# Kernel optimization log

Measured on AMD Instinct MI355X. Metric: run time of the kernel, lower is better.

The kernel has to match this reference:

```python
import jax, jax.numpy as jnp
import numpy as np
from jax import lax

N_QUBITS = 8
N_BLOCKS = 5

_H = jnp.array([[1.0, 1.0], [1.0, -1.0]], dtype=jnp.complex64) / np.sqrt(2.0).astype(np.float32)
# torchquantum PauliY.diagonalizing_gates = [Z, S, H] applied in order -> matrix H @ S @ Z = H @ diag(1, -1j)
_YROT = _H @ jnp.diag(jnp.array([1.0, -1j], dtype=jnp.complex64))


def apply_gate(st, U, wires):
    # st: [N, 2, 2, ..., 2] (n_qubits trailing axes); U: [2^k, 2^k]
    k = len(wires)
    axes = [w + 1 for w in wires]
    s = jnp.moveaxis(st, axes, list(range(1, k + 1)))
    shp = s.shape
    s = s.reshape(shp[0], 2 ** k, -1)
    s = jnp.einsum('ij,bjr->bir', U, s)
    return jnp.moveaxis(s.reshape(shp), list(range(1, k + 1)), axes)


def u3_mat(th, ph, lam):
    c = jnp.cos(0.5 * th).astype(jnp.complex64)
    s = jnp.sin(0.5 * th).astype(jnp.complex64)
    el = jnp.exp(1j * lam)
    ep = jnp.exp(1j * ph)
    return jnp.stack([jnp.stack([c, -el * s]), jnp.stack([ep * s, ep * el * c])])


def cu3_mat(th, ph, lam):
    M = jnp.eye(4, dtype=jnp.complex64)
    return M.at[2:, 2:].set(u3_mat(th, ph, lam))


def z_expvals(st):
    # <Z_w> for every wire from marginal probabilities
    n = st.ndim - 1
    mag = st.real ** 2 + st.imag ** 2
    outs = []
    for w in range(n):
        axes = tuple(a for a in range(1, n + 1) if a != w + 1)
        p = mag.sum(axes)  # [N, 2]
        outs.append(p[:, 0] - p[:, 1])
    return jnp.stack(outs, axis=1)


def quantum_conv(x, conv_w, conv_b, u3_params, cu3_params, fc_w, fc_b):
    n = N_QUBITS
    B, C, H, W = x.shape
    y = lax.conv_general_dilated(x, conv_w, (1, 1), 'SAME',
                                 dimension_numbers=('NCHW', 'OIHW', 'NCHW'))
    y = y + conv_b[None, :, None, None]
    ang = y.transpose(0, 2, 3, 1).reshape(-1, n)  # [B*H*W, n_qubits]
    Npx = ang.shape[0]
    # RY(theta)|0> encoding: product state of [cos(t/2), sin(t/2)] per wire
    c = jnp.cos(0.5 * ang)
    s = jnp.sin(0.5 * ang)
    st = jnp.stack([c[:, 0], s[:, 0]], axis=1).astype(jnp.complex64)
    for w in range(1, n):
        q = jnp.stack([c[:, w], s[:, w]], axis=1).astype(jnp.complex64)
        st = (st[:, :, None] * q[:, None, :]).reshape(Npx, -1)
    st = st.reshape((Npx,) + (2,) * n)
    # U3CU3Layer0: per block, U3 on each wire then circular CU3 ring
    for b in range(N_BLOCKS):
        for w in range(n):
            st = apply_gate(st, u3_mat(u3_params[b, w, 0], u3_params[b, w, 1], u3_params[b, w, 2]), [w])
        for w in range(n):
            st = apply_gate(st, cu3_mat(cu3_params[b, w, 0], cu3_params[b, w, 1], cu3_params[b, w, 2]), [w, (w + 1) % n])
    # MeasureAll(Z), then MeasureAll(X) and MeasureAll(Y) which MUTATE the device
    # state with their diagonalizing gates (torchquantum semantics)
    mz = z_expvals(st)
    for w in range(n):
        st = apply_gate(st, _H, [w])
    mx = z_expvals(st)
    for w in range(n):
        st = apply_gate(st, _YROT, [w])
    my = z_expvals(st)
    meas = jnp.concatenate([mz, mx, my], axis=1)  # [B*H*W, 3*n]
    out = meas @ fc_w.T + fc_b
    return out.reshape(B, H, W, -1).transpose(0, 3, 1, 2)


def setup_inputs() -> dict:
    key = jax.random.key(0)
    ks = jax.random.split(key, 7)
    n, cin, cout = N_QUBITS, 16, 32
    x = jax.random.normal(ks[0], (4, cin, 64, 64), dtype=jnp.float32)
    conv_w = jax.random.normal(ks[1], (n, cin, 3, 3), dtype=jnp.float32) / np.sqrt(cin * 9)
    conv_b = jax.random.normal(ks[2], (n,), dtype=jnp.float32) * 0.01
    u3_params = jax.random.uniform(ks[3], (N_BLOCKS, n, 3), dtype=jnp.float32, minval=-np.pi, maxval=np.pi)
    cu3_params = jax.random.uniform(ks[4], (N_BLOCKS, n, 3), dtype=jnp.float32, minval=-np.pi, maxval=np.pi)
    fc_w = jax.random.normal(ks[5], (cout, 3 * n), dtype=jnp.float32) / np.sqrt(3 * n)
    fc_b = jax.random.normal(ks[6], (cout,), dtype=jnp.float32) * 0.01
    return {'x': x, 'conv_w': conv_w, 'conv_b': conv_b, 'u3_params': u3_params,
            'cu3_params': cu3_params, 'fc_w': fc_w, 'fc_b': fc_b}


def reference(x, conv_w, conv_b, u3_params, cu3_params, fc_w, fc_b):
    return quantum_conv(x, conv_w, conv_b, u3_params, cu3_params, fc_w, fc_b)
```

## Files before the change

### kernel.cpp

```cpp
#include <hip/hip_runtime.h>

typedef float v2f __attribute__((ext_vector_type(2)));

template<int C>
__device__ __forceinline__ float dppmov(float x) {
  return __int_as_float(__builtin_amdgcn_update_dpp(0, __float_as_int(x), C, 0xF, 0xF, true));
}
template<int IMM>
__device__ __forceinline__ float dswz(float x) {
  return __int_as_float(__builtin_amdgcn_ds_swizzle(__float_as_int(x), IMM));
}
__device__ __forceinline__ float bperm(float x, int a) {
  return __int_as_float(__builtin_amdgcn_ds_bpermute(a, __float_as_int(x)));
}
template<int M>
__device__ __forceinline__ float bfly(float x) {
  if constexpr (M == 1)      return dppmov<0xB1>(x);
  else if constexpr (M == 2) return dppmov<0x4E>(x);
  else if constexpr (M == 3) return dppmov<0x1B>(x);
  else if constexpr (M == 8) return dppmov<0x128>(x);
  else                       return dswz<0x101F>(x);
}
template<int M>
__device__ __forceinline__ v2f bfly2(v2f v) {
  v2f o; o.x = bfly<M>(v.x); o.y = bfly<M>(v.y); return o;
}
__device__ __forceinline__ v2f sp(float s) { v2f v; v.x = s; v.y = s; return v; }
__device__ __forceinline__ v2f vfma(v2f a, v2f b, v2f c) {
  return __builtin_elementwise_fma(a, b, c);
}

template<int M, int CM>
__device__ __forceinline__ void crossG(v2f Sr[16], v2f Si[16],
    const float* g, int lane) {
  const bool hi = (lane & M) != 0;
  float fr, fi, gr, gi;
  if constexpr (CM == 0) {
    fr = hi ? g[6] : g[0]; fi = hi ? g[7] : g[1];
    gr = hi ? g[4] : g[2]; gi = hi ? g[5] : g[3];
  } else {
    const bool ct = (lane & CM) != 0;
    float f0r = hi ? g[6]  : g[0],  f0i = hi ? g[7]  : g[1];
    float g0r = hi ? g[4]  : g[2],  g0i = hi ? g[5]  : g[3];
    float f1r = hi ? g[14] : g[8],  f1i = hi ? g[15] : g[9];
    float g1r = hi ? g[12] : g[10], g1i = hi ? g[13] : g[11];
    fr = ct ? f1r : f0r; fi = ct ? f1i : f0i;
    gr = ct ? g1r : g0r; gi = ct ? g1i : g0i;
  }
  v2f vfr = sp(fr), vfi = sp(fi), vgr = sp(gr), vgi = sp(gi);
  v2f vfiN = sp(-fi), vgiN = sp(-gi);
#pragma unroll
  for (int r = 0; r < 16; ++r) {
    v2f pR = bfly2<M>(Sr[r]);
    v2f pI = bfly2<M>(Si[r]);
    v2f nR = vfma(vgiN, pI, vfma(vgr, pR, vfma(vfiN, Si[r], vfr * Sr[r])));
    v2f nI = vfma(vgi,  pR, vfma(vgr, pI, vfma(vfi,  Sr[r], vfr * Si[r])));
    Sr[r] = nR; Si[r] = nI;
  }
}

__device__ __forceinline__ void mixP(v2f& x0r, v2f& x0i, v2f& x1r, v2f& x1i,
    float m0r, float m0i, float m1r, float m1i,
    float m2r, float m2i, float m3r, float m3i) {
  v2f n0r = vfma(sp(-m1i), x1i, vfma(sp(m1r), x1r, vfma(sp(-m0i), x0i, sp(m0r) * x0r)));
  v2f n0i = vfma(sp( m1i), x1r, vfma(sp(m1r), x1i, vfma(sp( m0i), x0r, sp(m0r) * x0i)));
  v2f n1r = vfma(sp(-m3i), x1i, vfma(sp(m3r), x1r, vfma(sp(-m2i), x0i, sp(m2r) * x0r)));
  v2f n1i = vfma(sp( m3i), x1r, vfma(sp(m3r), x1i, vfma(sp( m2i), x0r, sp(m2r) * x0i)));
  x0r = n0r; x0i = n0i; x1r = n1r; x1i = n1i;
}

__device__ __forceinline__ void f23N(v2f Sr[16], v2f Si[16],
    const float* tab, int lane) {
  const int idx = ((lane >> 2) & 1) * 4 + (lane & 3);
  const float* rp = tab + idx * 8;
  const float c0r = rp[0], c0i = rp[1], c1r = rp[2], c1i = rp[3];
  const float c2r = rp[4], c2i = rp[5], c3r = rp[6], c3i = rp[7];
#pragma unroll
  for (int r = 0; r < 16; ++r) {
    v2f p1R = bfly2<1>(Sr[r]), p1I = bfly2<1>(Si[r]);
    v2f p2R = bfly2<2>(Sr[r]), p2I = bfly2<2>(Si[r]);
    v2f p3R = bfly2<3>(Sr[r]), p3I = bfly2<3>(Si[r]);
    v2f nR = sp(c0r) * Sr[r];
    nR = vfma(sp(-c0i), Si[r], nR);
    nR = vfma(sp( c1r), p1R, nR);  nR = vfma(sp(-c1i), p1I, nR);
    nR = vfma(sp( c2r), p2R, nR);  nR = vfma(sp(-c2i), p2I, nR);
    nR = vfma(sp( c3r), p3R, nR);  nR = vfma(sp(-c3i), p3I, nR);
    v2f nI = sp(c0i) * Sr[r];
    nI = vfma(sp(c0r), Si[r], nI);
    nI = vfma(sp(c1i), p1R, nI);   nI = vfma(sp(c1r), p1I, nI);
    nI = vfma(sp(c2i), p2R, nI);   nI = vfma(sp(c2r), p2I, nI);
    nI = vfma(sp(c3i), p3R, nI);   nI = vfma(sp(c3r), p3I, nI);
    Sr[r] = nR; Si[r] = nI;
  }
}

__device__ __forceinline__ void f4N(v2f Sr[16], v2f Si[16],
    const float* g, int lane) {
  const bool ct = (lane & 1) != 0;
  float m[8];
#pragma unroll
  for (int jj = 0; jj < 8; ++jj) m[jj] = ct ? g[8 + jj] : g[jj];
#pragma unroll
  for (int r = 0; r < 8; ++r)
    mixP(Sr[r], Si[r], Sr[r + 8], Si[r + 8],
         m[0], m[1], m[2], m[3], m[4], m[5], m[6], m[7]);
}
__device__ __forceinline__ void f5N(v2f Sr[16], v2f Si[16], const float* g) {
#pragma unroll
  for (int r = 0; r < 4; ++r)
    mixP(Sr[r], Si[r], Sr[r + 4], Si[r + 4],
         g[0], g[1], g[2], g[3], g[4], g[5], g[6], g[7]);
#pragma unroll
  for (int r = 8; r < 12; ++r)
    mixP(Sr[r], Si[r], Sr[r + 4], Si[r + 4],
         g[8], g[9], g[10], g[11], g[12], g[13], g[14], g[15]);
}
__device__ __forceinline__ void f67N(v2f Sr[16], v2f Si[16], const float* T) {
#pragma unroll
  for (int qd = 0; qd < 4; ++qd) {
    const int B = qd * 4;
    const float* M = T + (qd & 1) * 32;
    v2f ar0 = Sr[B+0], ai0 = Si[B+0], ar1 = Sr[B+1], ai1 = Si[B+1];
    v2f ar2 = Sr[B+2], ai2 = Si[B+2], ar3 = Sr[B+3], ai3 = Si[B+3];
#pragma unroll
    for (int rp = 0; rp < 4; ++rp) {
      const float* Mr = M + rp * 8;
      v2f nR = sp(Mr[0]) * ar0;
      nR = vfma(sp(-Mr[1]), ai0, nR);
      nR = vfma(sp( Mr[2]), ar1, nR);
      nR = vfma(sp(-Mr[3]), ai1, nR);
      nR = vfma(sp( Mr[4]), ar2, nR);
      nR = vfma(sp(-Mr[5]), ai2, nR);
      nR = vfma(sp( Mr[6]), ar3, nR);
      nR = vfma(sp(-Mr[7]), ai3, nR);
      v2f nI = sp(Mr[1]) * ar0;
      nI = vfma(sp(Mr[0]), ai0, nI);
      nI = vfma(sp(Mr[3]), ar1, nI);
      nI = vfma(sp(Mr[2]), ai1, nI);
      nI = vfma(sp(Mr[5]), ar2, nI);
      nI = vfma(sp(Mr[4]), ai2, nI);
      nI = vfma(sp(Mr[7]), ar3, nI);
      nI = vfma(sp(Mr[6]), ai3, nI);
      Sr[B + rp] = nR; Si[B + rp] = nI;
    }
  }
}
__device__ __forceinline__ void f8pN(v2f Sr[16], v2f Si[16],
    const float* g, int lane) {
  const bool hi = (lane & 8) != 0;
  float fr[2], fi[2], gr[2], gi[2];
  fr[0] = hi ? g[6]  : g[0];  fi[0] = hi ? g[7]  : g[1];
  gr[0] = hi ? g[4]  : g[2];  gi[0] = hi ? g[5]  : g[3];
  fr[1] = hi ? g[14] : g[8];  fi[1] = hi ? g[15] : g[9];
  gr[1] = hi ? g[12] : g[10]; gi[1] = hi ? g[13] : g[11];
#pragma unroll
  for (int r = 0; r < 16; ++r) {
    const int m = r & 1;
    v2f pR = bfly2<8>(Sr[r]);
    v2f pI = bfly2<8>(Si[r]);
    v2f nR = vfma(sp(-gi[m]), pI, vfma(sp(gr[m]), pR, vfma(sp(-fi[m]), Si[r], sp(fr[m]) * Sr[r])));
    v2f nI = vfma(sp( gi[m]), pR, vfma(sp(gr[m]), pI, vfma(sp( fi[m]), Sr[r], sp(fr[m]) * Si[r])));
    Sr[r] = nR; Si[r] = nI;
  }
}
__device__ __forceinline__ void f8N(v2f Sr[16], v2f Si[16],
    const float* g, int lane) {
  const bool hi = (lane & 8) != 0;
  const float fr = hi ? g[6] : g[0], fi = hi ? g[7] : g[1];
  const float gr = hi ? g[4] : g[2], gi = hi ? g[5] : g[3];
#pragma unroll
  for (int r = 1; r < 16; r += 2) {
    v2f pR = bfly2<8>(Sr[r]);
    v2f pI = bfly2<8>(Si[r]);
    v2f nR = vfma(sp(-gi), pI, vfma(sp(gr), pR, vfma(sp(-fi), Si[r], sp(fr) * Sr[r])));
    v2f nI = vfma(sp( gi), pR, vfma(sp(gr), pI, vfma(sp( fi), Sr[r], sp(fr) * Si[r])));
    Sr[r] = nR; Si[r] = nI;
  }
}

template<int M>
__device__ __forceinline__ void crossO(const v2f Sr[16], const v2f Si[16],
                                       v2f& re, v2f& im) {
  v2f r = sp(0.0f), i = sp(0.0f);
#pragma unroll
  for (int k = 0; k < 16; ++k) {
    v2f pr = bfly2<M>(Sr[k]);
    v2f pi = bfly2<M>(Si[k]);
    r = vfma(Sr[k], pr, r);
    r = vfma(Si[k], pi, r);
    i = vfma(Si[k], pr, i);
    i = vfma(-Sr[k], pi, i);
  }
  re = r; im = i;
}

__device__ __forceinline__ void mm2(const float* A, const float* B, float* D) {
  D[0] = A[0]*B[0] - A[1]*B[1] + A[2]*B[4] - A[3]*B[5];
  D[1] = A[0]*B[1] + A[1]*B[0] + A[2]*B[5] + A[3]*B[4];
  D[2] = A[0]*B[2] - A[1]*B[3] + A[2]*B[6] - A[3]*B[7];
  D[3] = A[0]*B[3] + A[1]*B[2] + A[2]*B[7] + A[3]*B[6];
  D[4] = A[4]*B[0] - A[5]*B[1] + A[6]*B[4] - A[7]*B[5];
  D[5] = A[4]*B[1] + A[5]*B[0] + A[6]*B[5] + A[7]*B[4];
  D[6] = A[4]*B[2] - A[5]*B[3] + A[6]*B[6] - A[7]*B[7];
  D[7] = A[4]*B[3] + A[5]*B[2] + A[6]*B[7] + A[7]*B[6];
}
__device__ __forceinline__ void u3fill(const float* src, float* o) {
  float th = src[0], ph = src[1], lam = src[2];
  float c = cosf(0.5f * th), s = sinf(0.5f * th);
  float cl = cosf(lam), sl = sinf(lam);
  float cp = cosf(ph), spv = sinf(ph);
  float cpl = cosf(ph + lam), spl = sinf(ph + lam);
  o[0] = c;        o[1] = 0.0f;
  o[2] = -cl * s;  o[3] = -sl * s;
  o[4] = cp * s;   o[5] = spv * s;
  o[6] = cpl * c;  o[7] = spl * c;
}

__global__ __launch_bounds__(256) void qconv_kernel(
    const float* __restrict__ x, const float* __restrict__ cw,
    const float* __restrict__ cb, const float* __restrict__ u3p,
    const float* __restrict__ cu3p, const float* __restrict__ fcw,
    const float* __restrict__ fcb, float* __restrict__ out) {
  __shared__ float Us[40][8];
  __shared__ float Cs[40][8];
  __shared__ float Gs[640];
  __shared__ float FCWs[768];
  __shared__ float F23t[320];
  __shared__ float F67t[320];

  {
    const int t = threadIdx.x;
    if (t < 40) u3fill(u3p + t * 3, Us[t]);
    if (t >= 64 && t < 104) u3fill(cu3p + (t - 64) * 3, Cs[t - 64]);
    for (int i = t; i < 768; i += 256) {
      int tt = i % 24;
      int stage = tt >> 3, w = tt & 7;
      float sc = (stage >= 1 && w >= 4) ? 2.0f : 1.0f;
      FCWs[i] = fcw[i] * sc;
    }
    __syncthreads();
    if (t == 0) {
#pragma unroll
      for (int j = 0; j < 8; ++j) Gs[j] = Us[0][j];
    } else if (t < 36) {
      int j = t - 1, b = j / 7, k = j % 7;
      float* dst = Gs + 8 + b * 112 + k * 16;
      const float* U = Us[b * 8 + k + 1];
      const float* C = Cs[b * 8 + k];
#pragma unroll
      for (int u = 0; u < 8; ++u) dst[u] = U[u];
      mm2(C, U, dst + 8);
    } else if (t < 40) {
      int b = t - 36;
      float* dst = Gs + 568 + b * 16;
      const float* U = Us[(b + 1) * 8];
      const float* C = Cs[b * 8 + 7];
#pragma unroll
      for (int u = 0; u < 8; ++u) dst[u] = U[u];
      mm2(U, C, dst + 8);
    } else if (t == 40) {
#pragma unroll
      for (int j = 0; j < 8; ++j) Gs[632 + j] = Cs[39][j];
    }
    __syncthreads();
    if (t < 40) {
      int b = t >> 3, idx = t & 7;
      int ct = idx >> 2, row = idx & 3;
      const float* M2 = Gs + 8 + b * 112 + 16 + ct * 8;
      int w2p = row >> 1, w3p = row & 1;
      const float* M3 = Gs + 8 + b * 112 + 32 + w2p * 8;
      float* dst = F23t + b * 64 + idx * 8;
#pragma unroll
      for (int k = 0; k < 4; ++k) {
        int w2 = w2p ^ (k >> 1), w3 = w3p ^ (k & 1);
        float a_r = M2[(w2p * 2 + w2) * 2], a_i = M2[(w2p * 2 + w2) * 2 + 1];
        float b_r = M3[(w3p * 2 + w3) * 2], b_i = M3[(w3p * 2 + w3) * 2 + 1];
        dst[k * 2]     = a_r * b_r - a_i * b_i;
        dst[k * 2 + 1] = a_r * b_i + a_i * b_r;
      }
    } else if (t >= 64 && t < 104) {
      int u = t - 64;
      int b = u >> 3, idx = u & 7;
      int ct = idx >> 2, rp = idx & 3;
      const float* M6 = Gs + 8 + b * 112 + 80 + ct * 8;
      int b1p = rp >> 1, b0p = rp & 1;
      const float* M7 = Gs + 8 + b * 112 + 96 + b1p * 8;
      float* dst = F67t + b * 64 + ct * 32 + rp * 8;
#pragma unroll
      for (int c = 0; c < 4; ++c) {
        int b1 = c >> 1, b0 = c & 1;
        float a_r = M6[(b1p * 2 + b1) * 2], a_i = M6[(b1p * 2 + b1) * 2 + 1];
        float b_r = M7[(b0p * 2 + b0) * 2], b_i = M7[(b0p * 2 + b0) * 2 + 1];
        dst[c * 2]     = a_r * b_r - a_i * b_i;
        dst[c * 2 + 1] = a_r * b_i + a_i * b_r;
      }
    }
    __syncthreads();
  }

  const int lane = threadIdx.x & 63;
  const int wid = __builtin_amdgcn_readfirstlane(
      (int)((blockIdx.x * blockDim.x + threadIdx.x) >> 6));
  const int p0 = wid * 8;
  const int q = lane & 15;

  float ang;
  {
    const int px = lane >> 3;
    const int oc = lane & 7;
    const int p  = p0 + px;
    const int b  = p >> 12;
    const int hh = (p >> 6) & 63;
    const int wim = p & 63;
    float acc = cb[oc];
#pragma unroll 4
    for (int ic = 0; ic < 16; ++ic) {
      const float* wp = cw + (oc * 16 + ic) * 9;
      const float* xp = x + (b * 16 + ic) * 4096;
#pragma unroll
      for (int kh = 0; kh < 3; ++kh) {
        int ih = hh + kh - 1;
        bool rok = (unsigned)ih < 64u;
        int ihc = rok ? ih : 0;
#pragma unroll
        for (int kw = 0; kw < 3; ++kw) {
          int iw = wim + kw - 1;
          bool ok = rok && ((unsigned)iw < 64u);
          int iwc = ((unsigned)iw < 64u) ? iw : 0;
          float xv = xp[ihc * 64 + iwc];
          acc = fmaf(ok ? xv : 0.0f, wp[kh * 3 + kw], acc);
        }
      }
    }
    ang = acc;
  }

  v2f Sr[16], Si[16];
  {
    const int gb = (lane & 48) << 2;
    float aA[8], aB[8];
#pragma unroll
    for (int w = 0; w < 8; ++w) {
      aA[w] = bperm(ang, gb + (w << 2));
      aB[w] = bperm(ang, gb + ((8 + w) << 2));
    }
    float cA[8], sA[8], cB[8], sB[8];
#pragma unroll
    for (int w = 0; w < 8; ++w) {
      __sincosf(0.5f * aA[w], &sA[w], &cA[w]);
      __sincosf(0.5f * aB[w], &sB[w], &cB[w]);
    }
    v2f c0; c0.x = cA[0]; c0.y = cB[0];
    v2f s0; s0.x = sA[0]; s0.y = sB[0];
    v2f c0r = vfma(sp(Gs[2]), s0, sp(Gs[0]) * c0);
    v2f c0i = vfma(sp(Gs[3]), s0, sp(Gs[1]) * c0);
    v2f s0r = vfma(sp(Gs[6]), s0, sp(Gs[4]) * c0);
    v2f s0i = vfma(sp(Gs[7]), s0, sp(Gs[5]) * c0);
    const bool w0 = (q & 8) != 0;
    v2f selR = w0 ? s0r : c0r;
    v2f selI = w0 ? s0i : c0i;
    float fA = ((q & 4) ? sA[1] : cA[1]) * ((q & 2) ? sA[2] : cA[2])
             * ((q & 1) ? sA[3] : cA[3]);
    float fB = ((q & 4) ? sB[1] : cB[1]) * ((q & 2) ? sB[2] : cB[2])
             * ((q & 1) ? sB[3] : cB[3]);
    v2f uu[4], vv[4];
    uu[0].x = cA[6]*cA[7]; uu[1].x = cA[6]*sA[7];
    uu[2].x = sA[6]*cA[7]; uu[3].x = sA[6]*sA[7];
    uu[0].y = cB[6]*cB[7]; uu[1].y = cB[6]*sB[7];
    uu[2].y = sB[6]*cB[7]; uu[3].y = sB[6]*sB[7];
    float vA0 = fA * cA[4], vA1 = fA * sA[4];
    float vB0 = fB * cB[4], vB1 = fB * sB[4];
    vv[0].x = vA0*cA[5]; vv[1].x = vA0*sA[5];
    vv[2].x = vA1*cA[5]; vv[3].x = vA1*sA[5];
    vv[0].y = vB0*cB[5]; vv[1].y = vB0*sB[5];
    vv[2].y = vB1*cB[5]; vv[3].y = vB1*sB[5];
#pragma unroll
    for (int r = 0; r < 16; ++r) {
      v2f base = vv[r >> 2] * uu[r & 3];
      Sr[r] = selR * base;
      Si[r] = selI * base;
    }
  }

  for (int b = 0; b < 5; ++b) {
    const float* base = Gs + 8 + b * 112;
    crossG<4, 8>(Sr, Si, base + 0, lane);
    f23N(Sr, Si, F23t + b * 64, lane);
    f4N(Sr, Si, base + 48, lane);
    f5N(Sr, Si, base + 64);
    f67N(Sr, Si, F67t + b * 64);
    if (b < 4) f8pN(Sr, Si, Gs + 568 + b * 16, lane);
  }
  f8N(Sr, Si, Gs + 632, lane);

  float sg[4];
  sg[0] = (q & 8) ? -1.0f : 1.0f;
  sg[1] = (q & 4) ? -1.0f : 1.0f;
  sg[2] = (q & 2) ? -1.0f : 1.0f;
  sg[3] = (q & 1) ? -1.0f : 1.0f;

  v2f PT[24];
  {
    v2f re0, im0, re1, im1, re2, im2, re3, im3;
    crossO<8>(Sr, Si, re0, im0);
    crossO<4>(Sr, Si, re1, im1);
    crossO<2>(Sr, Si, re2, im2);
    crossO<1>(Sr, Si, re3, im3);
    PT[8]  = re0; PT[9]  = re1; PT[10] = re2; PT[11] = re3;
    PT[16] = sp(sg[0]) * im0; PT[17] = sp(sg[1]) * im1;
    PT[18] = sp(sg[2]) * im2; PT[19] = sp(sg[3]) * im3;

    v2f P[16];
#pragma unroll
    for (int r = 0; r < 16; ++r) P[r] = vfma(Si[r], Si[r], Sr[r] * Sr[r]);
    v2f t01[8];
#pragma unroll
    for (int k = 0; k < 8; ++k) t01[k] = P[2*k] + P[2*k+1];
    v2f q0 = t01[0] + t01[1], q1 = t01[2] + t01[3];
    v2f q2 = t01[4] + t01[5], q3 = t01[6] + t01[7];
    v2f h0 = q0 + q1, h1 = q2 + q3;
    v2f p  = h0 + h1;
    PT[4] = h0 - h1;
    PT[5] = (q0 - q1) + (q2 - q3);
    PT[6] = (t01[0]-t01[1]) + (t01[2]-t01[3])
          + (t01[4]-t01[5]) + (t01[6]-t01[7]);
    PT[7] = (P[0]-P[1]) + (P[2]-P[3]) + (P[4]-P[5]) + (P[6]-P[7])
          + (P[8]-P[9]) + (P[10]-P[11]) + (P[12]-P[13]) + (P[14]-P[15]);
    PT[0] = sp(sg[0]) * p; PT[1] = sp(sg[1]) * p;
    PT[2] = sp(sg[2]) * p; PT[3] = sp(sg[3]) * p;

    v2f re, im;
    re = sp(0.0f); im = sp(0.0f);
#pragma unroll
    for (int r = 0; r < 8; ++r) {
      re = vfma(Sr[r], Sr[r+8], re); re = vfma(Si[r], Si[r+8], re);
      im = vfma(Si[r], Sr[r+8], im); im = vfma(-Sr[r], Si[r+8], im);
    }
    PT[12] = re; PT[20] = im;
    re = sp(0.0f); im = sp(0.0f);
#pragma unroll
    for (int t = 0; t < 8; ++t) {
      const int lo = (t & 3) + (t >> 2) * 8;
      re = vfma(Sr[lo], Sr[lo+4], re); re = vfma(Si[lo], Si[lo+4], re);
      im = vfma(Si[lo], Sr[lo+4], im); im = vfma(-Sr[lo], Si[lo+4], im);
    }
    PT[13] = re; PT[21] = im;
    re = sp(0.0f); im = sp(0.0f);
#pragma unroll
    for (int t = 0; t < 8; ++t) {
      const int lo = (t & 1) + (t >> 1) * 4;
      re = vfma(Sr[lo], Sr[lo+2], re); re = vfma(Si[lo], Si[lo+2], re);
      im = vfma(Si[lo], Sr[lo+2], im); im = vfma(-Sr[lo], Si[lo+2], im);
    }
    PT[14] = re; PT[22] = im;
    re = sp(0.0f); im = sp(0.0f);
#pragma unroll
    for (int t = 0; t < 8; ++t) {
      const int lo = 2 * t;
      re = vfma(Sr[lo], Sr[lo+1], re); re = vfma(Si[lo], Si[lo+1], re);
      im = vfma(Si[lo], Sr[lo+1], im); im = vfma(-Sr[lo], Si[lo+1], im);
    }
    PT[15] = re; PT[23] = im;
  }

  const int j = q & 7;
  const bool isB = (q & 8) != 0;
  float mm[24];
#pragma unroll
  for (int t = 0; t < 24; ++t) {
    v2f v = PT[t] + bfly2<8>(PT[t]);
    float s = isB ? v.y : v.x;
    s += bfly<1>(s);
    s += bfly<2>(s);
    s += bfly<4>(s);
    mm[t] = s;
  }

  const int g = lane >> 4;
  const int p = p0 + 2 * g + (isB ? 1 : 0);
  const int ob = (p >> 12) * 131072 + (p & 4095);
#pragma unroll
  for (int k = 0; k < 4; ++k) {
    const int ch = 4 * j + k;
    const float* wr = FCWs + ch * 24;
    float acc = fcb[ch];
#pragma unroll
    for (int u = 0; u < 24; ++u) acc = fmaf(mm[u], wr[u], acc);
    out[ob + ch * 4096] = acc;
  }
}

extern "C" void kernel_launch(void* const* d_in, const int* in_sizes, int n_in,
                              void* d_out, int out_size, void* d_ws, size_t ws_size,
                              hipStream_t stream) {
  const float* x      = (const float*)d_in[0];
  const float* conv_w = (const float*)d_in[1];
  const float* conv_b = (const float*)d_in[2];
  const float* u3p    = (const float*)d_in[3];
  const float* cu3p   = (const float*)d_in[4];
  const float* fcw    = (const float*)d_in[5];
  const float* fcb    = (const float*)d_in[6];
  float* out = (float*)d_out;

  qconv_kernel<<<512, 256, 0, stream>>>(x, conv_w, conv_b, u3p, cu3p,
                                        fcw, fcb, out);
}
```

Before: 106.4 us.

## Split gate-matrix prep into separate kernel and read gate tables from global memory

```diff
diff --git a/kernel.cpp b/kernel.cpp
--- a/kernel.cpp
+++ b/kernel.cpp
@@ -32,21 +32,15 @@
 
 template<int M, int CM>
 __device__ __forceinline__ void crossG(v2f Sr[16], v2f Si[16],
-    const float* g, int lane) {
+    const float* __restrict__ g, int lane) {
   const bool hi = (lane & M) != 0;
-  float fr, fi, gr, gi;
-  if constexpr (CM == 0) {
-    fr = hi ? g[6] : g[0]; fi = hi ? g[7] : g[1];
-    gr = hi ? g[4] : g[2]; gi = hi ? g[5] : g[3];
-  } else {
-    const bool ct = (lane & CM) != 0;
-    float f0r = hi ? g[6]  : g[0],  f0i = hi ? g[7]  : g[1];
-    float g0r = hi ? g[4]  : g[2],  g0i = hi ? g[5]  : g[3];
-    float f1r = hi ? g[14] : g[8],  f1i = hi ? g[15] : g[9];
-    float g1r = hi ? g[12] : g[10], g1i = hi ? g[13] : g[11];
-    fr = ct ? f1r : f0r; fi = ct ? f1i : f0i;
-    gr = ct ? g1r : g0r; gi = ct ? g1i : g0i;
-  }
+  const bool ct = (lane & CM) != 0;
+  float f0r = hi ? g[6]  : g[0],  f0i = hi ? g[7]  : g[1];
+  float g0r = hi ? g[4]  : g[2],  g0i = hi ? g[5]  : g[3];
+  float f1r = hi ? g[14] : g[8],  f1i = hi ? g[15] : g[9];
+  float g1r = hi ? g[12] : g[10], g1i = hi ? g[13] : g[11];
+  float fr = ct ? f1r : f0r, fi = ct ? f1i : f0i;
+  float gr = ct ? g1r : g0r, gi = ct ? g1i : g0i;
   v2f vfr = sp(fr), vfi = sp(fi), vgr = sp(gr), vgi = sp(gi);
   v2f vfiN = sp(-fi), vgiN = sp(-gi);
 #pragma unroll
@@ -69,33 +63,8 @@
   x0r = n0r; x0i = n0i; x1r = n1r; x1i = n1i;
 }
 
-__device__ __forceinline__ void f23N(v2f Sr[16], v2f Si[16],
-    const float* tab, int lane) {
-  const int idx = ((lane >> 2) & 1) * 4 + (lane & 3);
-  const float* rp = tab + idx * 8;
-  const float c0r = rp[0], c0i = rp[1], c1r = rp[2], c1i = rp[3];
-  const float c2r = rp[4], c2i = rp[5], c3r = rp[6], c3i = rp[7];
-#pragma unroll
-  for (int r = 0; r < 16; ++r) {
-    v2f p1R = bfly2<1>(Sr[r]), p1I = bfly2<1>(Si[r]);
-    v2f p2R = bfly2<2>(Sr[r]), p2I = bfly2<2>(Si[r]);
-    v2f p3R = bfly2<3>(Sr[r]), p3I = bfly2<3>(Si[r]);
-    v2f nR = sp(c0r) * Sr[r];
-    nR = vfma(sp(-c0i), Si[r], nR);
-    nR = vfma(sp( c1r), p1R, nR);  nR = vfma(sp(-c1i), p1I, nR);
-    nR = vfma(sp( c2r), p2R, nR);  nR = vfma(sp(-c2i), p2I, nR);
-    nR = vfma(sp( c3r), p3R, nR);  nR = vfma(sp(-c3i), p3I, nR);
-    v2f nI = sp(c0i) * Sr[r];
-    nI = vfma(sp(c0r), Si[r], nI);
-    nI = vfma(sp(c1i), p1R, nI);   nI = vfma(sp(c1r), p1I, nI);
-    nI = vfma(sp(c2i), p2R, nI);   nI = vfma(sp(c2r), p2I, nI);
-    nI = vfma(sp(c3i), p3R, nI);   nI = vfma(sp(c3r), p3I, nI);
-    Sr[r] = nR; Si[r] = nI;
-  }
-}
-
 __device__ __forceinline__ void f4N(v2f Sr[16], v2f Si[16],
-    const float* g, int lane) {
+    const float* __restrict__ g, int lane) {
   const bool ct = (lane & 1) != 0;
   float m[8];
 #pragma unroll
@@ -105,7 +74,8 @@
     mixP(Sr[r], Si[r], Sr[r + 8], Si[r + 8],
          m[0], m[1], m[2], m[3], m[4], m[5], m[6], m[7]);
 }
-__device__ __forceinline__ void f5N(v2f Sr[16], v2f Si[16], const float* g) {
+__device__ __forceinline__ void f5N(v2f Sr[16], v2f Si[16],
+    const float* __restrict__ g) {
 #pragma unroll
   for (int r = 0; r < 4; ++r)
     mixP(Sr[r], Si[r], Sr[r + 4], Si[r + 4],
@@ -115,16 +85,17 @@
     mixP(Sr[r], Si[r], Sr[r + 4], Si[r + 4],
          g[8], g[9], g[10], g[11], g[12], g[13], g[14], g[15]);
 }
-__device__ __forceinline__ void f67N(v2f Sr[16], v2f Si[16], const float* T) {
+__device__ __forceinline__ void f67N(v2f Sr[16], v2f Si[16],
+    const float* __restrict__ T) {
 #pragma unroll
   for (int qd = 0; qd < 4; ++qd) {
     const int B = qd * 4;
-    const float* M = T + (qd & 1) * 32;
+    const float* __restrict__ M = T + (qd & 1) * 32;
     v2f ar0 = Sr[B+0], ai0 = Si[B+0], ar1 = Sr[B+1], ai1 = Si[B+1];
     v2f ar2 = Sr[B+2], ai2 = Si[B+2], ar3 = Sr[B+3], ai3 = Si[B+3];
 #pragma unroll
     for (int rp = 0; rp < 4; ++rp) {
-      const float* Mr = M + rp * 8;
+      const float* __restrict__ Mr = M + rp * 8;
       v2f nR = sp(Mr[0]) * ar0;
       nR = vfma(sp(-Mr[1]), ai0, nR);
       nR = vfma(sp( Mr[2]), ar1, nR);
@@ -146,7 +117,7 @@
   }
 }
 __device__ __forceinline__ void f8pN(v2f Sr[16], v2f Si[16],
-    const float* g, int lane) {
+    const float* __restrict__ g, int lane) {
   const bool hi = (lane & 8) != 0;
   float fr[2], fi[2], gr[2], gi[2];
   fr[0] = hi ? g[6]  : g[0];  fi[0] = hi ? g[7]  : g[1];
@@ -164,7 +135,7 @@
   }
 }
 __device__ __forceinline__ void f8N(v2f Sr[16], v2f Si[16],
-    const float* g, int lane) {
+    const float* __restrict__ g, int lane) {
   const bool hi = (lane & 8) != 0;
   const float fr = hi ? g[6] : g[0], fi = hi ? g[7] : g[1];
   const float gr = hi ? g[4] : g[2], gi = hi ? g[5] : g[3];
@@ -216,87 +187,76 @@
   o[6] = cpl * c;  o[7] = spl * c;
 }
 
-__global__ __launch_bounds__(256) void qconv_kernel(
-    const float* __restrict__ x, const float* __restrict__ cw,
-    const float* __restrict__ cb, const float* __restrict__ u3p,
-    const float* __restrict__ cu3p, const float* __restrict__ fcw,
-    const float* __restrict__ fcb, float* __restrict__ out) {
+__global__ __launch_bounds__(256) void qprep_kernel(
+    const float* __restrict__ u3p, const float* __restrict__ cu3p,
+    const float* __restrict__ fcw, float* __restrict__ ws) {
   __shared__ float Us[40][8];
   __shared__ float Cs[40][8];
   __shared__ float Gs[640];
-  __shared__ float FCWs[768];
-  __shared__ float F23t[320];
-  __shared__ float F67t[320];
-
-  {
-    const int t = threadIdx.x;
-    if (t < 40) u3fill(u3p + t * 3, Us[t]);
-    if (t >= 64 && t < 104) u3fill(cu3p + (t - 64) * 3, Cs[t - 64]);
-    for (int i = t; i < 768; i += 256) {
-      int tt = i % 24;
-      int stage = tt >> 3, w = tt & 7;
-      float sc = (stage >= 1 && w >= 4) ? 2.0f : 1.0f;
-      FCWs[i] = fcw[i] * sc;
-    }
-    __syncthreads();
-    if (t == 0) {
-#pragma unroll
-      for (int j = 0; j < 8; ++j) Gs[j] = Us[0][j];
-    } else if (t < 36) {
-      int j = t - 1, b = j / 7, k = j % 7;
-      float* dst = Gs + 8 + b * 112 + k * 16;
-      const float* U = Us[b * 8 + k + 1];
-      const float* C = Cs[b * 8 + k];
-#pragma unroll
-      for (int u = 0; u < 8; ++u) dst[u] = U[u];
-      mm2(C, U, dst + 8);
-    } else if (t < 40) {
-      int b = t - 36;
-      float* dst = Gs + 568 + b * 16;
-      const float* U = Us[(b + 1) * 8];
-      const float* C = Cs[b * 8 + 7];
-#pragma unroll
-      for (int u = 0; u < 8; ++u) dst[u] = U[u];
-      mm2(U, C, dst + 8);
-    } else if (t == 40) {
-#pragma unroll
-      for (int j = 0; j < 8; ++j) Gs[632 + j] = Cs[39][j];
-    }
-    __syncthreads();
-    if (t < 40) {
-      int b = t >> 3, idx = t & 7;
-      int ct = idx >> 2, row = idx & 3;
-      const float* M2 = Gs + 8 + b * 112 + 16 + ct * 8;
-      int w2p = row >> 1, w3p = row & 1;
-      const float* M3 = Gs + 8 + b * 112 + 32 + w2p * 8;
-      float* dst = F23t + b * 64 + idx * 8;
-#pragma unroll
-      for (int k = 0; k < 4; ++k) {
-        int w2 = w2p ^ (k >> 1), w3 = w3p ^ (k & 1);
-        float a_r = M2[(w2p * 2 + w2) * 2], a_i = M2[(w2p * 2 + w2) * 2 + 1];
-        float b_r = M3[(w3p * 2 + w3) * 2], b_i = M3[(w3p * 2 + w3) * 2 + 1];
-        dst[k * 2]     = a_r * b_r - a_i * b_i;
-        dst[k * 2 + 1] = a_r * b_i + a_i * b_r;
-      }
-    } else if (t >= 64 && t < 104) {
-      int u = t - 64;
-      int b = u >> 3, idx = u & 7;
-      int ct = idx >> 2, rp = idx & 3;
-      const float* M6 = Gs + 8 + b * 112 + 80 + ct * 8;
-      int b1p = rp >> 1, b0p = rp & 1;
-      const float* M7 = Gs + 8 + b * 112 + 96 + b1p * 8;
-      float* dst = F67t + b * 64 + ct * 32 + rp * 8;
-#pragma unroll
-      for (int c = 0; c < 4; ++c) {
-        int b1 = c >> 1, b0 = c & 1;
-        float a_r = M6[(b1p * 2 + b1) * 2], a_i = M6[(b1p * 2 + b1) * 2 + 1];
-        float b_r = M7[(b0p * 2 + b0) * 2], b_i = M7[(b0p * 2 + b0) * 2 + 1];
-        dst[c * 2]     = a_r * b_r - a_i * b_i;
-        dst[c * 2 + 1] = a_r * b_i + a_i * b_r;
-      }
-    }
-    __syncthreads();
-  }
+  const int t = threadIdx.x;
+  if (t < 40) u3fill(u3p + t * 3, Us[t]);
+  if (t >= 64 && t < 104) u3fill(cu3p + (t - 64) * 3, Cs[t - 64]);
+  __syncthreads();
+  if (t == 0) {
+#pragma unroll
+    for (int j = 0; j < 8; ++j) Gs[j] = Us[0][j];
+  } else if (t < 36) {
+    int j = t - 1, b = j / 7, k = j % 7;
+    float* dst = Gs + 8 + b * 112 + k * 16;
+    const float* U = Us[b * 8 + k + 1];
+    const float* C = Cs[b * 8 + k];
+#pragma unroll
+    for (int u = 0; u < 8; ++u) dst[u] = U[u];
+    mm2(C, U, dst + 8);
+  } else if (t < 40) {
+    int b = t - 36;
+    float* dst = Gs + 568 + b * 16;
+    const float* U = Us[(b + 1) * 8];
+    const float* C = Cs[b * 8 + 7];
+#pragma unroll
+    for (int u = 0; u < 8; ++u) dst[u] = U[u];
+    mm2(U, C, dst + 8);
+  } else if (t == 40) {
+#pragma unroll
+    for (int j = 0; j < 8; ++j) Gs[632 + j] = Cs[39][j];
+  }
+  __syncthreads();
+  if (t >= 64 && t < 104) {
+    int u = t - 64;
+    int b = u >> 3, idx = u & 7;
+    int ct = idx >> 2, rp = idx & 3;
+    const float* M6 = Gs + 8 + b * 112 + 80 + ct * 8;
+    int b1p = rp >> 1, b0p = rp & 1;
+    const float* M7 = Gs + 8 + b * 112 + 96 + b1p * 8;
+    float* dst = ws + 1536 + b * 64 + ct * 32 + rp * 8;
+#pragma unroll
+    for (int c = 0; c < 4; ++c) {
+      int b1 = c >> 1, b0 = c & 1;
+      float a_r = M6[(b1p * 2 + b1) * 2], a_i = M6[(b1p * 2 + b1) * 2 + 1];
+      float b_r = M7[(b0p * 2 + b0) * 2], b_i = M7[(b0p * 2 + b0) * 2 + 1];
+      dst[c * 2]     = a_r * b_r - a_i * b_i;
+      dst[c * 2 + 1] = a_r * b_i + a_i * b_r;
+    }
+  }
+  for (int i = t; i < 32 * 28; i += 256) {
+    int ch = i / 28, u = i - ch * 28;
+    float v = 0.0f;
+    if (u < 24) {
+      float sc = (u >= 8 && (u & 7) >= 4) ? 2.0f : 1.0f;
+      v = fcw[ch * 24 + u] * sc;
+    }
+    ws[640 + i] = v;
+  }
+  for (int i = t; i < 640; i += 256) ws[i] = Gs[i];
+}
+
+__global__ __launch_bounds__(256) void qconv_kernel(
+    const float* __restrict__ x, const float* __restrict__ cw,
+    const float* __restrict__ cb, const float* __restrict__ fcb,
+    const float* __restrict__ wsc, float* __restrict__ out) {
+  __shared__ float FCWs[32 * 28];
+  for (int i = threadIdx.x; i < 32 * 28; i += 256) FCWs[i] = wsc[640 + i];
+  __syncthreads();
 
   const int lane = threadIdx.x & 63;
   const int wid = __builtin_amdgcn_readfirstlane(
@@ -352,10 +312,10 @@
     }
     v2f c0; c0.x = cA[0]; c0.y = cB[0];
     v2f s0; s0.x = sA[0]; s0.y = sB[0];
-    v2f c0r = vfma(sp(Gs[2]), s0, sp(Gs[0]) * c0);
-    v2f c0i = vfma(sp(Gs[3]), s0, sp(Gs[1]) * c0);
-    v2f s0r = vfma(sp(Gs[6]), s0, sp(Gs[4]) * c0);
-    v2f s0i = vfma(sp(Gs[7]), s0, sp(Gs[5]) * c0);
+    v2f c0r = vfma(sp(wsc[2]), s0, sp(wsc[0]) * c0);
+    v2f c0i = vfma(sp(wsc[3]), s0, sp(wsc[1]) * c0);
+    v2f s0r = vfma(sp(wsc[6]), s0, sp(wsc[4]) * c0);
+    v2f s0i = vfma(sp(wsc[7]), s0, sp(wsc[5]) * c0);
     const bool w0 = (q & 8) != 0;
     v2f selR = w0 ? s0r : c0r;
     v2f selI = w0 ? s0i : c0i;
@@ -383,15 +343,16 @@
   }
 
   for (int b = 0; b < 5; ++b) {
-    const float* base = Gs + 8 + b * 112;
+    const float* __restrict__ base = wsc + 8 + b * 112;
     crossG<4, 8>(Sr, Si, base + 0, lane);
-    f23N(Sr, Si, F23t + b * 64, lane);
+    crossG<2, 4>(Sr, Si, base + 16, lane);
+    crossG<1, 2>(Sr, Si, base + 32, lane);
     f4N(Sr, Si, base + 48, lane);
     f5N(Sr, Si, base + 64);
-    f67N(Sr, Si, F67t + b * 64);
-    if (b < 4) f8pN(Sr, Si, Gs + 568 + b * 16, lane);
-  }
-  f8N(Sr, Si, Gs + 632, lane);
+    f67N(Sr, Si, wsc + 1536 + b * 64);
+    if (b < 4) f8pN(Sr, Si, wsc + 568 + b * 16, lane);
+  }
+  f8N(Sr, Si, wsc + 632, lane);
 
   float sg[4];
   sg[0] = (q & 8) ? -1.0f : 1.0f;
@@ -482,7 +443,7 @@
 #pragma unroll
   for (int k = 0; k < 4; ++k) {
     const int ch = 4 * j + k;
-    const float* wr = FCWs + ch * 24;
+    const float* wr = FCWs + ch * 28;
     float acc = fcb[ch];
 #pragma unroll
     for (int u = 0; u < 24; ++u) acc = fmaf(mm[u], wr[u], acc);
@@ -501,7 +462,8 @@
   const float* fcw    = (const float*)d_in[5];
   const float* fcb    = (const float*)d_in[6];
   float* out = (float*)d_out;
-
-  qconv_kernel<<<512, 256, 0, stream>>>(x, conv_w, conv_b, u3p, cu3p,
-                                        fcw, fcb, out);
-}
+  float* ws  = (float*)d_ws;
+
+  qprep_kernel<<<1, 256, 0, stream>>>(u3p, cu3p, fcw, ws);
+  qconv_kernel<<<512, 256, 0, stream>>>(x, conv_w, conv_b, fcb, ws, out);
+}
```

After: 112.7 us. 1.06x slower.
